# Optimization experiments

Hardware: AMD Instinct MI355X
Metric: run time of the kernel (lower is better)

The kernel has to match this reference:

```python
import jax, jax.numpy as jnp
import numpy as np

B, C, H, W, E, R, TOP_K = 8, 128, 128, 128, 4, 64, 2


def setup_inputs() -> dict:
    key = jax.random.key(0)
    ks = jax.random.split(key, 12)
    s = 0.02
    return {
        "x": jax.random.normal(ks[0], (B, C, H, W), jnp.float32),
        "shared": jax.random.normal(ks[1], (B, C, H, W), jnp.float32),
        # FrequencyEmbedding MLP: Linear(C,2C) -> GELU -> Linear(2C,C)
        "mlp_w1": jax.random.normal(ks[2], (C, 2 * C), jnp.float32) * s,
        "mlp_b1": jnp.zeros((2 * C,), jnp.float32),
        "mlp_w2": jax.random.normal(ks[3], (2 * C, C), jnp.float32) * s,
        "mlp_b2": jnp.zeros((C,), jnp.float32),
        # routing gates: Linear(C,E) on pooled x, Linear(C,E) on freq emb
        "gate_w": jax.random.normal(ks[4], (C, E), jnp.float32) * s,
        "freq_gate_w": jax.random.normal(ks[5], (C, E), jnp.float32) * s,
        # per-expert 1x1 conv weights (ModExpert.proj, expert_layer=Identity)
        "exp_w0": jax.random.normal(ks[6], (E, R, C), jnp.float32) * s,  # dim->rank
        "exp_w1": jax.random.normal(ks[7], (E, R, C), jnp.float32) * s,  # dim->rank (on shared)
        "exp_w2": jax.random.normal(ks[8], (E, C, R), jnp.float32) * s,  # rank->dim
        # AdapterLayer.proj_out 1x1 conv
        "proj_w": jax.random.normal(ks[9], (C, C), jnp.float32) * s,
    }


def reference(x, shared, mlp_w1, mlp_b1, mlp_w2, mlp_b2, gate_w, freq_gate_w,
              exp_w0, exp_w1, exp_w2, proj_w):
    b, c = x.shape[0], x.shape[1]
    # --- FrequencyEmbedding: frozen depthwise high-pass 3x3 -> GELU -> mean(HW) -> MLP ---
    hp = jnp.array([[-1., -1., -1.], [-1., 8., -1.], [-1., -1., -1.]], dtype=x.dtype)
    kern = jnp.broadcast_to(hp, (c, 1, 3, 3))
    h = jax.lax.conv_general_dilated(
        x, kern, window_strides=(1, 1), padding='SAME',
        feature_group_count=c, dimension_numbers=('NCHW', 'OIHW', 'NCHW'))
    h = jax.nn.gelu(h, approximate=False)
    fe = h.mean(axis=(-2, -1))                                    # [B, C]
    fe = jax.nn.gelu(fe @ mlp_w1 + mlp_b1, approximate=False) @ mlp_w2 + mlp_b2
    # --- RoutingFunction (eval / noiseless): softmax -> top-k -> scatter gates ---
    pooled = x.mean(axis=(-2, -1))                                # [B, C]
    logits = pooled @ gate_w + fe @ freq_gate_w                   # [B, E]
    scores = jax.nn.softmax(logits, axis=-1)
    vals, idx = jax.lax.top_k(scores, TOP_K)
    gates = jnp.zeros_like(scores).at[jnp.arange(b)[:, None], idx].set(vals)  # [B, E]
    # --- Experts (dense equivalent of SparseDispatcher gather->expert->scatter-add) ---
    # expert_e(x, shared) = x + W2_e @ ((W0_e @ x) * silu(W1_e @ shared))
    a = jnp.einsum('bchw,erc->berhw', x, exp_w0)                  # [B,E,R,H,W]
    g = jax.nn.silu(jnp.einsum('bchw,erc->berhw', shared, exp_w1))
    y = jnp.einsum('berhw,edr->bedhw', a * g, exp_w2)             # [B,E,C,H,W]
    # gated combine; residual shortcut enters once per selected expert, weighted by gate
    out = jnp.einsum('be,bedhw->bdhw', gates, y) + gates.sum(axis=1)[:, None, None, None] * x
    # --- proj_out 1x1 ---
    return jnp.einsum('bchw,dc->bdhw', out, proj_w)
```

## Files before the change

### kernel.cpp

```cpp
#include <hip/hip_runtime.h>
#include <hip/hip_bf16.h>
#include <math.h>

#define CC   128
#define HWN  16384
#define EE   4
#define RR   64
#define TP   64
#define NT   (HWN / TP)

typedef __attribute__((ext_vector_type(8))) short short8;
typedef __attribute__((ext_vector_type(4))) float f32x4;

__device__ __forceinline__ unsigned short f2bf(float f) {
    __hip_bfloat16 h = __float2bfloat16(f);
    return *reinterpret_cast<unsigned short*>(&h);
}
__device__ __forceinline__ unsigned pk2bf(float lo, float hi) {
    return (unsigned)f2bf(lo) | ((unsigned)f2bf(hi) << 16);
}
__device__ __forceinline__ float gelu_exact(float v) {
    return 0.5f * v * (1.0f + erff(v * 0.7071067811865475f));
}
__device__ __forceinline__ float silu_f(float v) {
    return v / (1.0f + expf(-v));
}

#define PREP_CONV 1024
#define PREP_WCV  (PREP_CONV + 128)
#define PREP_WF   (PREP_WCV + 128)
#define PREP_GRID (PREP_WF + 48)
__global__ __launch_bounds__(256, 4) void k_prep(
    const float* __restrict__ x,   const float* __restrict__ sh,
    const float* __restrict__ proj,
    const float* __restrict__ ew0, const float* __restrict__ ew1,
    const float* __restrict__ ew2,
    const float* __restrict__ mw1, const float* __restrict__ mw2,
    const float* __restrict__ gw,  const float* __restrict__ fgw,
    float* __restrict__ fe0p, float* __restrict__ poolp,
    unsigned short* __restrict__ projb, unsigned short* __restrict__ w0b,
    unsigned short* __restrict__ w1b,   unsigned short* __restrict__ w2pb,
    float* __restrict__ outw, float* __restrict__ dummy)
{
    __shared__ float wr[8][4];
    const int bx = blockIdx.x, tid = threadIdx.x;

    if (bx < PREP_CONV) {
        const int b    = bx >> 7;
        const int dpr  = (bx & 127) >> 1;
        const int band = bx & 1;
        const int ln   = tid & 63;
        const int wv   = tid >> 6;
        const int half = ln >> 5;
        const int l    = ln & 31;
        const int c4   = l << 2;
        const int strm = wv * 2 + half;
        const int r0   = band * 64 + strm * 8;

        const float* srcA = x + ((size_t)(b * CC + 2 * dpr)) * HWN + c4;
        const float* srcB = srcA + HWN;
        unsigned* dst = (unsigned*)outw + ((size_t)(b * CC + dpr)) * HWN + c4;

        const float4 z4 = {0.f, 0.f, 0.f, 0.f};
        float4 tA = z4, tB = z4, mA, mB, bA = z4, bB = z4;
        float tlA = 0.f, trA = 0.f, tlB = 0.f, trB = 0.f;
        float mlA, mrA, mlB, mrB, blA = 0.f, brA = 0.f, blB = 0.f, brB = 0.f;
        if (r0 > 0) {
            tA = *(const float4*)(srcA + (size_t)(r0 - 1) * 128);
            tB = *(const float4*)(srcB + (size_t)(r0 - 1) * 128);
            tlA = __shfl(tA.w, ln - 1, 64); if (l == 0)  tlA = 0.f;
            trA = __shfl(tA.x, ln + 1, 64); if (l == 31) trA = 0.f;
            tlB = __shfl(tB.w, ln - 1, 64); if (l == 0)  tlB = 0.f;
            trB = __shfl(tB.x, ln + 1, 64); if (l == 31) trB = 0.f;
        }
        mA = *(const float4*)(srcA + (size_t)r0 * 128);
        mB = *(const float4*)(srcB + (size_t)r0 * 128);
        mlA = __shfl(mA.w, ln - 1, 64); if (l == 0)  mlA = 0.f;
        mrA = __shfl(mA.x, ln + 1, 64); if (l == 31) mrA = 0.f;
        mlB = __shfl(mB.w, ln - 1, 64); if (l == 0)  mlB = 0.f;
        mrB = __shfl(mB.x, ln + 1, 64); if (l == 31) mrB = 0.f;

        float sgA = 0.f, sxA = 0.f, sgB = 0.f, sxB = 0.f;
        for (int g = r0; g < r0 + 8; ++g) {
            if (g + 1 < 128) {
                bA = *(const float4*)(srcA + (size_t)(g + 1) * 128);
                bB = *(const float4*)(srcB + (size_t)(g + 1) * 128);
                blA = __shfl(bA.w, ln - 1, 64); if (l == 0)  blA = 0.f;
                brA = __shfl(bA.x, ln + 1, 64); if (l == 31) brA = 0.f;
                blB = __shfl(bB.w, ln - 1, 64); if (l == 0)  blB = 0.f;
                brB = __shfl(bB.x, ln + 1, 64); if (l == 31) brB = 0.f;
            } else { bA = z4; bB = z4; blA = brA = blB = brB = 0.f; }
            {
                const float ta[6] = {tlA, tA.x, tA.y, tA.z, tA.w, trA};
                const float ma[6] = {mlA, mA.x, mA.y, mA.z, mA.w, mrA};
                const float ba[6] = {blA, bA.x, bA.y, bA.z, bA.w, brA};
                #pragma unroll
                for (int k = 0; k < 4; ++k) {
                    float s8 = ((ta[k] + ta[k+1]) + (ta[k+2] + ma[k]))
                             + ((ma[k+2] + ba[k]) + (ba[k+1] + ba[k+2]));
                    sgA += gelu_exact(8.f * ma[k+1] - s8);
                    sxA += ma[k+1];
                }
            }
            {
                const float ta[6] = {tlB, tB.x, tB.y, tB.z, tB.w, trB};
                const float ma[6] = {mlB, mB.x, mB.y, mB.z, mB.w, mrB};
                const float ba[6] = {blB, bB.x, bB.y, bB.z, bB.w, brB};
                #pragma unroll
                for (int k = 0; k < 4; ++k) {
                    float s8 = ((ta[k] + ta[k+1]) + (ta[k+2] + ma[k]))
                             + ((ma[k+2] + ba[k]) + (ba[k+1] + ba[k+2]));
                    sgB += gelu_exact(8.f * ma[k+1] - s8);
                    sxB += ma[k+1];
                }
            }
            uint4 w;
            w.x = pk2bf(mA.x, mB.x); w.y = pk2bf(mA.y, mB.y);
            w.z = pk2bf(mA.z, mB.z); w.w = pk2bf(mA.w, mB.w);
            *(uint4*)(dst + (size_t)g * 128) = w;
            tA = mA; tlA = mlA; trA = mrA; mA = bA; mlA = blA; mrA = brA;
            tB = mB; tlB = mlB; trB = mrB; mB = bB; mlB = blB; mrB = brB;
        }
        #pragma unroll
        for (int off = 16; off; off >>= 1) {
            sgA += __shfl_xor(sgA, off, 64); sxA += __shfl_xor(sxA, off, 64);
            sgB += __shfl_xor(sgB, off, 64); sxB += __shfl_xor(sxB, off, 64);
        }
        if (l == 0) { wr[strm][0] = sgA; wr[strm][1] = sxA; wr[strm][2] = sgB; wr[strm][3] = sxB; }
        __syncthreads();
        if (tid < 4) {
            float s = 0.f;
            #pragma unroll
            for (int q = 0; q < 8; ++q) s += wr[q][tid];
            s *= (1.f / 16384.f);
            const int o = band * 1024 + b * CC + 2 * dpr;
            if (tid == 0) fe0p [o]     = s;
            if (tid == 1) poolp[o]     = s;
            if (tid == 2) fe0p [o + 1] = s;
            if (tid == 3) poolp[o + 1] = s;
        }
        {
            const float4* a4  = (const float4*)(sh + ((size_t)(b * CC + 2 * dpr)) * HWN + band * 8192);
            const float4* c4p = (const float4*)(sh + ((size_t)(b * CC + 2 * dpr + 1)) * HWN + band * 8192);
            uint4* dsts = (uint4*)((unsigned*)outw + ((size_t)(b * CC + 64 + dpr)) * HWN + band * 8192);
            for (int i = tid; i < 2048; i += 256) {
                float4 a = a4[i], c = c4p[i];
                uint4 w;
                w.x = pk2bf(a.x, c.x); w.y = pk2bf(a.y, c.y);
                w.z = pk2bf(a.z, c.z); w.w = pk2bf(a.w, c.w);
                dsts[i] = w;
            }
        }
    } else if (bx < PREP_WCV) {
        int i = (bx - PREP_CONV) * 256 + tid;
        if (i < CC * CC) projb[i] = f2bf(proj[i]);
        w0b[i] = f2bf(ew0[i]);
        w1b[i] = f2bf(ew1[i]);
    } else if (bx < PREP_WF) {
        const int bb = bx - PREP_WCV;
        const int e  = bb >> 5;
        const int d  = ((bb & 31) << 2) + (tid >> 6);
        const int r  = tid & 63;
        const float* pr = proj + d * CC;
        const float* wz = ew2 + (size_t)e * CC * RR + r;
        float a0 = 0.f, a1 = 0.f, a2 = 0.f, a3 = 0.f;
        for (int c = 0; c < CC; c += 4) {
            a0 += pr[c + 0] * wz[(c + 0) * RR];
            a1 += pr[c + 1] * wz[(c + 1) * RR];
            a2 += pr[c + 2] * wz[(c + 2) * RR];
            a3 += pr[c + 3] * wz[(c + 3) * RR];
        }
        w2pb[(e * CC + d) * RR + r] = f2bf((a0 + a1) + (a2 + a3));
    } else {
        const int i = (bx - PREP_WF) * 256 + tid;
        float s = 0.f;
        for (int j = i; j < CC * 2 * CC; j += 48 * 256) s += mw1[j] + mw2[j];
        if (i < CC * EE) s += gw[i] + fgw[i];
        if (s == 12345.678f) dummy[1] = s;
    }
}

__global__ __launch_bounds__(256) void k_route(
    const float* __restrict__ fe0p, const float* __restrict__ poolp,
    const float* __restrict__ w1, const float* __restrict__ b1,
    const float* __restrict__ w2, const float* __restrict__ b2,
    const float* __restrict__ gw, const float* __restrict__ fgw,
    float* __restrict__ gates, float* __restrict__ gsum)
{
    const int b = blockIdx.x, tid = threadIdx.x;
    __shared__ float hh[256];
    __shared__ float fe[128];
    __shared__ float lg[4];
    {
        const float* f0 = fe0p + b * CC;
        const float* f1 = fe0p + 1024 + b * CC;
        float a[8];
        #pragma unroll
        for (int j = 0; j < 8; ++j) a[j] = 0.f;
        for (int c = 0; c < CC; c += 8)
            #pragma unroll
            for (int j = 0; j < 8; ++j) a[j] += (f0[c + j] + f1[c + j]) * w1[(c + j) * 256 + tid];
        float acc = b1[tid] + ((a[0]+a[1]) + (a[2]+a[3])) + ((a[4]+a[5]) + (a[6]+a[7]));
        hh[tid] = gelu_exact(acc);
    }
    __syncthreads();
    if (tid < 128) {
        float a[8];
        #pragma unroll
        for (int j = 0; j < 8; ++j) a[j] = 0.f;
        for (int c = 0; c < 256; c += 8)
            #pragma unroll
            for (int j = 0; j < 8; ++j) a[j] += hh[c + j] * w2[(c + j) * 128 + tid];
        fe[tid] = b2[tid] + ((a[0]+a[1]) + (a[2]+a[3])) + ((a[4]+a[5]) + (a[6]+a[7]));
    }
    __syncthreads();
    if (tid < EE) {
        const float* pl0 = poolp + b * CC;
        const float* pl1 = poolp + 1024 + b * CC;
        float l0=0.f, l1=0.f, l2=0.f, l3=0.f;
        for (int c = 0; c < CC; c += 4) {
            l0 += (pl0[c+0]+pl1[c+0]) * gw[(c+0) * EE + tid] + fe[c+0] * fgw[(c+0) * EE + tid];
            l1 += (pl0[c+1]+pl1[c+1]) * gw[(c+1) * EE + tid] + fe[c+1] * fgw[(c+1) * EE + tid];
            l2 += (pl0[c+2]+pl1[c+2]) * gw[(c+2) * EE + tid] + fe[c+2] * fgw[(c+2) * EE + tid];
            l3 += (pl0[c+3]+pl1[c+3]) * gw[(c+3) * EE + tid] + fe[c+3] * fgw[(c+3) * EE + tid];
        }
        lg[tid] = (l0 + l1) + (l2 + l3);
    }
    __syncthreads();
    if (tid == 0) {
        float mx = fmaxf(fmaxf(lg[0], lg[1]), fmaxf(lg[2], lg[3]));
        float sc[EE]; float ssum = 0.f;
        for (int e = 0; e < EE; ++e) { sc[e] = expf(lg[e] - mx); ssum += sc[e]; }
        float inv = 1.f / ssum;
        for (int e = 0; e < EE; ++e) sc[e] *= inv;
        int i1 = 0;
        for (int e = 1; e < EE; ++e) if (sc[e] > sc[i1]) i1 = e;
        int i2 = -1;
        for (int e = 0; e < EE; ++e) {
            if (e == i1) continue;
            if (i2 < 0 || sc[e] > sc[i2]) i2 = e;
        }
        for (int e = 0; e < EE; ++e)
            gates[b * EE + e] = (e == i1) ? sc[i1] : (e == i2 ? sc[i2] : 0.f);
        gsum[b] = sc[i1] + sc[i2];
    }
}

__global__ __launch_bounds__(256, 4) void k_experts(
    const unsigned short* __restrict__ w0b, const unsigned short* __restrict__ w1b,
    const unsigned short* __restrict__ w2pb, const unsigned short* __restrict__ projb,
    const float* __restrict__ gates, const float* __restrict__ gsum,
    float* __restrict__ out)
{
    __shared__ __align__(16) unsigned short xs [TP * CC];
    __shared__ __align__(16) unsigned short shs[TP * CC];
    __shared__ __align__(16) unsigned short us [TP * RR];
    const int tid  = threadIdx.x;
    const int b    = blockIdx.x >> 8;
    const int tile = blockIdx.x & (NT - 1);
    const int p0   = tile * TP;

    {
        const unsigned* wsrc = (const unsigned*)out + ((size_t)b * CC) * HWN + p0;
        const int p  = tid & 63;
        const int qh = tid >> 6;
        #pragma unroll
        for (int it = 0; it < 4; ++it) {
            const int q  = it * 4 + qh;
            const int sw = p * CC + ((q ^ (p & 15)) << 3);
            const unsigned* px_ = wsrc + (size_t)(q * 4) * HWN + p;
            const unsigned* ps_ = wsrc + (size_t)(64 + q * 4) * HWN + p;
            uint4 wx, wh;
            wx.x = px_[0]; wx.y = px_[HWN]; wx.z = px_[2 * HWN]; wx.w = px_[3 * HWN];
            wh.x = ps_[0]; wh.y = ps_[HWN]; wh.z = ps_[2 * HWN]; wh.w = ps_[3 * HWN];
            *(uint4*)&xs [sw] = wx;
            *(uint4*)&shs[sw] = wh;
        }
    }
    __syncthreads();

    const int wv = tid >> 6;
    const int ln = tid & 63;
    const int lp = ln & 15;
    const int lq = ln >> 4;

    f32x4 acc[2][4];
    #pragma unroll
    for (int i = 0; i < 2; ++i)
        #pragma unroll
        for (int j = 0; j < 4; ++j) acc[i][j] = (f32x4){0.f, 0.f, 0.f, 0.f};

    {
        const int d0 = wv * 32;
        #pragma unroll
        for (int ks = 0; ks < 4; ++ks) {
            const int k0 = ks * 32 + lq * 8;
            const int ch = ks * 4 + lq;
            short8 a0 = *(const short8*)&projb[(d0 +      lp) * CC + k0];
            short8 a1 = *(const short8*)&projb[(d0 + 16 + lp) * CC + k0];
            #pragma unroll
            for (int pt = 0; pt < 4; ++pt) {
                short8 bf = *(const short8*)&xs[(pt * 16 + lp) * CC + ((ch ^ lp) << 3)];
                acc[0][pt] = __builtin_amdgcn_mfma_f32_16x16x32_bf16(a0, bf, acc[0][pt], 0, 0, 0);
                acc[1][pt] = __builtin_amdgcn_mfma_f32_16x16x32_bf16(a1, bf, acc[1][pt], 0, 0, 0);
            }
        }
        const float gs = gsum[b];
        #pragma unroll
        for (int i = 0; i < 2; ++i)
            #pragma unroll
            for (int j = 0; j < 4; ++j) acc[i][j] *= gs;
    }

    for (int e = 0; e < EE; ++e) {
        const float ge = gates[b * EE + e];
        if (ge == 0.f) continue;

        f32x4 af[4], gf[4];
        #pragma unroll
        for (int pt = 0; pt < 4; ++pt) { af[pt] = (f32x4){0.f,0.f,0.f,0.f}; gf[pt] = (f32x4){0.f,0.f,0.f,0.f}; }
        const unsigned short* w0e = w0b + (size_t)(e * RR + wv * 16) * CC;
        const unsigned short* w1e = w1b + (size_t)(e * RR + wv * 16) * CC;
        #pragma unroll
        for (int ks = 0; ks < 4; ++ks) {
            const int k0 = ks * 32 + lq * 8;
            const int ch = ks * 4 + lq;
            short8 a0 = *(const short8*)&w0e[lp * CC + k0];
            short8 a1 = *(const short8*)&w1e[lp * CC + k0];
            #pragma unroll
            for (int pt = 0; pt < 4; ++pt) {
                const int sw = (pt * 16 + lp) * CC + ((ch ^ lp) << 3);
                short8 bx = *(const short8*)&xs [sw];
                short8 bs = *(const short8*)&shs[sw];
                af[pt] = __builtin_amdgcn_mfma_f32_16x16x32_bf16(a0, bx, af[pt], 0, 0, 0);
                gf[pt] = __builtin_amdgcn_mfma_f32_16x16x32_bf16(a1, bs, gf[pt], 0, 0, 0);
            }
        }
        __syncthreads();
        #pragma unroll
        for (int pt = 0; pt < 4; ++pt) {
            unsigned short t[4];
            #pragma unroll
            for (int i = 0; i < 4; ++i)
                t[i] = f2bf(ge * af[pt][i] * silu_f(gf[pt][i]));
            const int p = pt * 16 + lp;
            const int addr = p * RR + (((wv * 2 + (lq >> 1)) ^ (lp & 7)) << 3) + ((lq & 1) << 2);
            *(uint2*)&us[addr] = *(uint2*)t;
        }
        __syncthreads();
        const unsigned short* w2e = w2pb + (size_t)(e * CC + wv * 32) * RR;
        #pragma unroll
        for (int ks = 0; ks < 2; ++ks) {
            const int k0 = ks * 32 + lq * 8;
            const int ch = ks * 4 + lq;
            short8 a0 = *(const short8*)&w2e[lp * RR + k0];
            short8 a1 = *(const short8*)&w2e[(16 + lp) * RR + k0];
            #pragma unroll
            for (int pt = 0; pt < 4; ++pt) {
                short8 bu = *(const short8*)&us[(pt * 16 + lp) * RR + ((ch ^ (lp & 7)) << 3)];
                acc[0][pt] = __builtin_amdgcn_mfma_f32_16x16x32_bf16(a0, bu, acc[0][pt], 0, 0, 0);
                acc[1][pt] = __builtin_amdgcn_mfma_f32_16x16x32_bf16(a1, bu, acc[1][pt], 0, 0, 0);
            }
        }
    }

    {
        const int d0 = wv * 32;
        #pragma unroll
        for (int dt = 0; dt < 2; ++dt)
            #pragma unroll
            for (int pt = 0; pt < 4; ++pt) {
                float* ob = out + ((size_t)(b * CC + d0 + dt * 16 + lq * 4)) * HWN + p0 + pt * 16 + lp;
                #pragma unroll
                for (int i = 0; i < 4; ++i)
                    ob[(size_t)i * HWN] = acc[dt][pt][i];
            }
    }
}

extern "C" void kernel_launch(void* const* d_in, const int* in_sizes, int n_in,
                              void* d_out, int out_size, void* d_ws, size_t ws_size,
                              hipStream_t stream) {
    const float* x    = (const float*)d_in[0];
    const float* shr  = (const float*)d_in[1];
    const float* mw1  = (const float*)d_in[2];
    const float* mb1  = (const float*)d_in[3];
    const float* mw2  = (const float*)d_in[4];
    const float* mb2  = (const float*)d_in[5];
    const float* gw   = (const float*)d_in[6];
    const float* fgw  = (const float*)d_in[7];
    const float* ew0  = (const float*)d_in[8];
    const float* ew1  = (const float*)d_in[9];
    const float* ew2  = (const float*)d_in[10];
    const float* pw   = (const float*)d_in[11];
    float* out = (float*)d_out;

    float* ws     = (float*)d_ws;
    float* fe0p   = ws + 0;
    float* poolp  = ws + 2048;
    float* gates  = ws + 4096;
    float* gsum   = ws + 4128;
    float* dummy  = ws + 4136;
    unsigned short* projb = (unsigned short*)(ws + 4160);
    unsigned short* w0b   = projb + 16384;
    unsigned short* w1b   = w0b + 32768;
    unsigned short* w2pb  = w1b + 32768;

    k_prep   <<<PREP_GRID, 256, 0, stream>>>(x, shr, pw, ew0, ew1, ew2, mw1, mw2,
                                             gw, fgw, fe0p, poolp, projb, w0b, w1b, w2pb,
                                             out, dummy);
    k_route  <<<8,         256, 0, stream>>>(fe0p, poolp, mw1, mb1, mw2, mb2, gw, fgw, gates, gsum);
    k_experts<<<8 * NT,    256, 0, stream>>>(w0b, w1b, w2pb, projb, gates, gsum, out);
}
```

Measured before the change: 253.8 us.

## Split prep stencil into four row bands with float2 per-lane columns

The prep kernel's high-pass/GELU/pooling stage now splits each channel pair into four row bands instead of two, doubling the conv block count. Each lane handles two columns across a full 128-wide row, and halo columns come from direct loads rather than shuffles. The shared-tensor bf16 conversion moves ahead of the barrier, and the routing kernel sums four partials instead of two. The goal is more parallelism and better latency hiding in this memory-bound stage, at the cost of narrower loads, redundant halo reads and an enlarged workspace layout.

After: 263.8 us. +4.0%, slower.

```diff
diff --git a/kernel.cpp b/kernel.cpp
--- a/kernel.cpp
+++ b/kernel.cpp
@@ -26,11 +26,11 @@
     return v / (1.0f + expf(-v));
 }
 
-#define PREP_CONV 1024
+#define PREP_CONV 2048
 #define PREP_WCV  (PREP_CONV + 128)
 #define PREP_WF   (PREP_WCV + 128)
 #define PREP_GRID (PREP_WF + 48)
-__global__ __launch_bounds__(256, 4) void k_prep(
+__global__ __launch_bounds__(256) void k_prep(
     const float* __restrict__ x,   const float* __restrict__ sh,
     const float* __restrict__ proj,
     const float* __restrict__ ew0, const float* __restrict__ ew1,
@@ -42,114 +42,109 @@
     unsigned short* __restrict__ w1b,   unsigned short* __restrict__ w2pb,
     float* __restrict__ outw, float* __restrict__ dummy)
 {
-    __shared__ float wr[8][4];
+    __shared__ float wr[4][4];
     const int bx = blockIdx.x, tid = threadIdx.x;
 
     if (bx < PREP_CONV) {
-        const int b    = bx >> 7;
-        const int dpr  = (bx & 127) >> 1;
-        const int band = bx & 1;
+        const int b    = bx >> 8;
+        const int dpr  = (bx >> 2) & 63;
+        const int band = bx & 3;
         const int ln   = tid & 63;
         const int wv   = tid >> 6;
-        const int half = ln >> 5;
-        const int l    = ln & 31;
-        const int c4   = l << 2;
-        const int strm = wv * 2 + half;
-        const int r0   = band * 64 + strm * 8;
-
-        const float* srcA = x + ((size_t)(b * CC + 2 * dpr)) * HWN + c4;
+        const int c0   = ln << 1;
+        const int r0   = band * 32 + wv * 8;
+
+        const float* srcA = x + ((size_t)(b * CC + 2 * dpr)) * HWN;
         const float* srcB = srcA + HWN;
-        unsigned* dst = (unsigned*)outw + ((size_t)(b * CC + dpr)) * HWN + c4;
-
-        const float4 z4 = {0.f, 0.f, 0.f, 0.f};
-        float4 tA = z4, tB = z4, mA, mB, bA = z4, bB = z4;
-        float tlA = 0.f, trA = 0.f, tlB = 0.f, trB = 0.f;
-        float mlA, mrA, mlB, mrB, blA = 0.f, brA = 0.f, blB = 0.f, brB = 0.f;
+        unsigned* dst = (unsigned*)outw + ((size_t)(b * CC + dpr)) * HWN;
+
+        const bool le = (c0 == 0), re = (c0 == 126);
+        const int cl = le ? 0 : c0 - 1;
+        const int cr = re ? 127 : c0 + 2;
+
+        const float2 z2 = {0.f, 0.f};
+        float2 tA, tB, mA, mB;
+        float tlA, trA, tlB, trB, mlA, mrA, mlB, mrB;
         if (r0 > 0) {
-            tA = *(const float4*)(srcA + (size_t)(r0 - 1) * 128);
-            tB = *(const float4*)(srcB + (size_t)(r0 - 1) * 128);
-            tlA = __shfl(tA.w, ln - 1, 64); if (l == 0)  tlA = 0.f;
-            trA = __shfl(tA.x, ln + 1, 64); if (l == 31) trA = 0.f;
-            tlB = __shfl(tB.w, ln - 1, 64); if (l == 0)  tlB = 0.f;
-            trB = __shfl(tB.x, ln + 1, 64); if (l == 31) trB = 0.f;
-        }
-        mA = *(const float4*)(srcA + (size_t)r0 * 128);
-        mB = *(const float4*)(srcB + (size_t)r0 * 128);
-        mlA = __shfl(mA.w, ln - 1, 64); if (l == 0)  mlA = 0.f;
-        mrA = __shfl(mA.x, ln + 1, 64); if (l == 31) mrA = 0.f;
-        mlB = __shfl(mB.w, ln - 1, 64); if (l == 0)  mlB = 0.f;
-        mrB = __shfl(mB.x, ln + 1, 64); if (l == 31) mrB = 0.f;
+            const float* rA = srcA + (size_t)(r0 - 1) * 128;
+            const float* rB = srcB + (size_t)(r0 - 1) * 128;
+            tA = *(const float2*)(rA + c0);
+            tB = *(const float2*)(rB + c0);
+            tlA = le ? 0.f : rA[cl]; trA = re ? 0.f : rA[cr];
+            tlB = le ? 0.f : rB[cl]; trB = re ? 0.f : rB[cr];
+        } else { tA = z2; tB = z2; tlA = trA = tlB = trB = 0.f; }
+        {
+            const float* rA = srcA + (size_t)r0 * 128;
+            const float* rB = srcB + (size_t)r0 * 128;
+            mA = *(const float2*)(rA + c0);
+            mB = *(const float2*)(rB + c0);
+            mlA = le ? 0.f : rA[cl]; mrA = re ? 0.f : rA[cr];
+            mlB = le ? 0.f : rB[cl]; mrB = re ? 0.f : rB[cr];
+        }
 
         float sgA = 0.f, sxA = 0.f, sgB = 0.f, sxB = 0.f;
-        for (int g = r0; g < r0 + 8; ++g) {
-            if (g + 1 < 128) {
-                bA = *(const float4*)(srcA + (size_t)(g + 1) * 128);
-                bB = *(const float4*)(srcB + (size_t)(g + 1) * 128);
-                blA = __shfl(bA.w, ln - 1, 64); if (l == 0)  blA = 0.f;
-                brA = __shfl(bA.x, ln + 1, 64); if (l == 31) brA = 0.f;
-                blB = __shfl(bB.w, ln - 1, 64); if (l == 0)  blB = 0.f;
-                brB = __shfl(bB.x, ln + 1, 64); if (l == 31) brB = 0.f;
-            } else { bA = z4; bB = z4; blA = brA = blB = brB = 0.f; }
+        #pragma unroll
+        for (int g = 0; g < 8; ++g) {
+            const int gr = r0 + g;
+            float2 bA, bB; float blA, brA, blB, brB;
+            if (gr + 1 < 128) {
+                const float* rA = srcA + (size_t)(gr + 1) * 128;
+                const float* rB = srcB + (size_t)(gr + 1) * 128;
+                bA = *(const float2*)(rA + c0);
+                bB = *(const float2*)(rB + c0);
+                blA = le ? 0.f : rA[cl]; brA = re ? 0.f : rA[cr];
+                blB = le ? 0.f : rB[cl]; brB = re ? 0.f : rB[cr];
+            } else { bA = z2; bB = z2; blA = brA = blB = brB = 0.f; }
             {
-                const float ta[6] = {tlA, tA.x, tA.y, tA.z, tA.w, trA};
-                const float ma[6] = {mlA, mA.x, mA.y, mA.z, mA.w, mrA};
-                const float ba[6] = {blA, bA.x, bA.y, bA.z, bA.w, brA};
-                #pragma unroll
-                for (int k = 0; k < 4; ++k) {
-                    float s8 = ((ta[k] + ta[k+1]) + (ta[k+2] + ma[k]))
-                             + ((ma[k+2] + ba[k]) + (ba[k+1] + ba[k+2]));
-                    sgA += gelu_exact(8.f * ma[k+1] - s8);
-                    sxA += ma[k+1];
-                }
+                float s8 = ((tlA + tA.x) + (tA.y + mlA)) + ((mA.y + blA) + (bA.x + bA.y));
+                sgA += gelu_exact(8.f * mA.x - s8);
+                s8 = ((tA.x + tA.y) + (trA + mA.x)) + ((mrA + bA.x) + (bA.y + brA));
+                sgA += gelu_exact(8.f * mA.y - s8);
+                sxA += mA.x + mA.y;
             }
             {
-                const float ta[6] = {tlB, tB.x, tB.y, tB.z, tB.w, trB};
-                const float ma[6] = {mlB, mB.x, mB.y, mB.z, mB.w, mrB};
-                const float ba[6] = {blB, bB.x, bB.y, bB.z, bB.w, brB};
-                #pragma unroll
-                for (int k = 0; k < 4; ++k) {
-                    float s8 = ((ta[k] + ta[k+1]) + (ta[k+2] + ma[k]))
-                             + ((ma[k+2] + ba[k]) + (ba[k+1] + ba[k+2]));
-                    sgB += gelu_exact(8.f * ma[k+1] - s8);
-                    sxB += ma[k+1];
-                }
-            }
-            uint4 w;
-            w.x = pk2bf(mA.x, mB.x); w.y = pk2bf(mA.y, mB.y);
-            w.z = pk2bf(mA.z, mB.z); w.w = pk2bf(mA.w, mB.w);
-            *(uint4*)(dst + (size_t)g * 128) = w;
+                float s8 = ((tlB + tB.x) + (tB.y + mlB)) + ((mB.y + blB) + (bB.x + bB.y));
+                sgB += gelu_exact(8.f * mB.x - s8);
+                s8 = ((tB.x + tB.y) + (trB + mB.x)) + ((mrB + bB.x) + (bB.y + brB));
+                sgB += gelu_exact(8.f * mB.y - s8);
+                sxB += mB.x + mB.y;
+            }
+            uint2 w;
+            w.x = pk2bf(mA.x, mB.x);
+            w.y = pk2bf(mA.y, mB.y);
+            *(uint2*)(dst + (size_t)gr * 128 + c0) = w;
             tA = mA; tlA = mlA; trA = mrA; mA = bA; mlA = blA; mrA = brA;
             tB = mB; tlB = mlB; trB = mrB; mB = bB; mlB = blB; mrB = brB;
         }
         #pragma unroll
-        for (int off = 16; off; off >>= 1) {
+        for (int off = 32; off; off >>= 1) {
             sgA += __shfl_xor(sgA, off, 64); sxA += __shfl_xor(sxA, off, 64);
             sgB += __shfl_xor(sgB, off, 64); sxB += __shfl_xor(sxB, off, 64);
         }
-        if (l == 0) { wr[strm][0] = sgA; wr[strm][1] = sxA; wr[strm][2] = sgB; wr[strm][3] = sxB; }
+        if (ln == 0) { wr[wv][0] = sgA; wr[wv][1] = sxA; wr[wv][2] = sgB; wr[wv][3] = sxB; }
+        {
+            const float4* a4  = (const float4*)(sh + ((size_t)(b * CC + 2 * dpr)) * HWN + band * 4096);
+            const float4* c4p = (const float4*)(sh + ((size_t)(b * CC + 2 * dpr + 1)) * HWN + band * 4096);
+            uint4* dsts = (uint4*)((unsigned*)outw + ((size_t)(b * CC + 64 + dpr)) * HWN + band * 4096);
+            #pragma unroll
+            for (int it = 0; it < 4; ++it) {
+                const int i = it * 256 + tid;
+                float4 a = a4[i], c = c4p[i];
+                uint4 w;
+                w.x = pk2bf(a.x, c.x); w.y = pk2bf(a.y, c.y);
+                w.z = pk2bf(a.z, c.z); w.w = pk2bf(a.w, c.w);
+                dsts[i] = w;
+            }
+        }
         __syncthreads();
         if (tid < 4) {
-            float s = 0.f;
-            #pragma unroll
-            for (int q = 0; q < 8; ++q) s += wr[q][tid];
+            float s = (wr[0][tid] + wr[1][tid]) + (wr[2][tid] + wr[3][tid]);
             s *= (1.f / 16384.f);
             const int o = band * 1024 + b * CC + 2 * dpr;
             if (tid == 0) fe0p [o]     = s;
             if (tid == 1) poolp[o]     = s;
             if (tid == 2) fe0p [o + 1] = s;
             if (tid == 3) poolp[o + 1] = s;
-        }
-        {
-            const float4* a4  = (const float4*)(sh + ((size_t)(b * CC + 2 * dpr)) * HWN + band * 8192);
-            const float4* c4p = (const float4*)(sh + ((size_t)(b * CC + 2 * dpr + 1)) * HWN + band * 8192);
-            uint4* dsts = (uint4*)((unsigned*)outw + ((size_t)(b * CC + 64 + dpr)) * HWN + band * 8192);
-            for (int i = tid; i < 2048; i += 256) {
-                float4 a = a4[i], c = c4p[i];
-                uint4 w;
-                w.x = pk2bf(a.x, c.x); w.y = pk2bf(a.y, c.y);
-                w.z = pk2bf(a.z, c.z); w.w = pk2bf(a.w, c.w);
-                dsts[i] = w;
-            }
         }
     } else if (bx < PREP_WCV) {
         int i = (bx - PREP_CONV) * 256 + tid;
@@ -193,13 +188,16 @@
     __shared__ float lg[4];
     {
         const float* f0 = fe0p + b * CC;
-        const float* f1 = fe0p + 1024 + b * CC;
         float a[8];
         #pragma unroll
         for (int j = 0; j < 8; ++j) a[j] = 0.f;
         for (int c = 0; c < CC; c += 8)
             #pragma unroll
-            for (int j = 0; j < 8; ++j) a[j] += (f0[c + j] + f1[c + j]) * w1[(c + j) * 256 + tid];
+            for (int j = 0; j < 8; ++j) {
+                const int cc = c + j;
+                float v = (f0[cc] + f0[1024 + cc]) + (f0[2048 + cc] + f0[3072 + cc]);
+                a[j] += v * w1[cc * 256 + tid];
+            }
         float acc = b1[tid] + ((a[0]+a[1]) + (a[2]+a[3])) + ((a[4]+a[5]) + (a[6]+a[7]));
         hh[tid] = gelu_exact(acc);
     }
@@ -215,14 +213,17 @@
     }
     __syncthreads();
     if (tid < EE) {
-        const float* pl0 = poolp + b * CC;
-        const float* pl1 = poolp + 1024 + b * CC;
+        const float* pl = poolp + b * CC;
         float l0=0.f, l1=0.f, l2=0.f, l3=0.f;
         for (int c = 0; c < CC; c += 4) {
-            l0 += (pl0[c+0]+pl1[c+0]) * gw[(c+0) * EE + tid] + fe[c+0] * fgw[(c+0) * EE + tid];
-            l1 += (pl0[c+1]+pl1[c+1]) * gw[(c+1) * EE + tid] + fe[c+1] * fgw[(c+1) * EE + tid];
-            l2 += (pl0[c+2]+pl1[c+2]) * gw[(c+2) * EE + tid] + fe[c+2] * fgw[(c+2) * EE + tid];
-            l3 += (pl0[c+3]+pl1[c+3]) * gw[(c+3) * EE + tid] + fe[c+3] * fgw[(c+3) * EE + tid];
+            float p0 = (pl[c+0] + pl[1024+c+0]) + (pl[2048+c+0] + pl[3072+c+0]);
+            float p1 = (pl[c+1] + pl[1024+c+1]) + (pl[2048+c+1] + pl[3072+c+1]);
+            float p2 = (pl[c+2] + pl[1024+c+2]) + (pl[2048+c+2] + pl[3072+c+2]);
+            float p3 = (pl[c+3] + pl[1024+c+3]) + (pl[2048+c+3] + pl[3072+c+3]);
+            l0 += p0 * gw[(c+0) * EE + tid] + fe[c+0] * fgw[(c+0) * EE + tid];
+            l1 += p1 * gw[(c+1) * EE + tid] + fe[c+1] * fgw[(c+1) * EE + tid];
+            l2 += p2 * gw[(c+2) * EE + tid] + fe[c+2] * fgw[(c+2) * EE + tid];
+            l3 += p3 * gw[(c+3) * EE + tid] + fe[c+3] * fgw[(c+3) * EE + tid];
         }
         lg[tid] = (l0 + l1) + (l2 + l3);
     }
@@ -397,11 +398,11 @@
 
     float* ws     = (float*)d_ws;
     float* fe0p   = ws + 0;
-    float* poolp  = ws + 2048;
-    float* gates  = ws + 4096;
-    float* gsum   = ws + 4128;
-    float* dummy  = ws + 4136;
-    unsigned short* projb = (unsigned short*)(ws + 4160);
+    float* poolp  = ws + 4096;
+    float* gates  = ws + 8192;
+    float* gsum   = ws + 8224;
+    float* dummy  = ws + 8232;
+    unsigned short* projb = (unsigned short*)(ws + 8256);
     unsigned short* w0b   = projb + 16384;
     unsigned short* w1b   = w0b + 32768;
     unsigned short* w2pb  = w1b + 32768;
```
